# Performance work log

Hardware: AMD Instinct MI355X
Metric: run time of the kernel (lower is better)

## Reference

```python
import jax, jax.numpy as jnp
import numpy as np

D_MODEL = 1024
N_HEADS = 16
D_HEAD = D_MODEL // N_HEADS
NEG_INF = -1000000000.0


def setup_inputs() -> dict:
    key = jax.random.key(0)
    ks = jax.random.split(key, 12)
    B, S1, S2 = 2, 2048, 2048
    query = jax.random.normal(ks[0], (B, S1, D_MODEL), dtype=jnp.float32)
    k_in = jax.random.normal(ks[1], (B, S2, D_MODEL), dtype=jnp.float32)
    v_in = jax.random.normal(ks[2], (B, S2, D_MODEL), dtype=jnp.float32)
    # causal mask: True = position is masked out (filled with -1e9)
    mask = jnp.broadcast_to(jnp.triu(jnp.ones((S1, S2), dtype=bool), k=1), (B, S1, S2))
    s = 1.0 / np.sqrt(D_MODEL)
    W_q = jax.random.uniform(ks[3], (D_MODEL, D_MODEL), jnp.float32, -s, s)
    b_q = jax.random.uniform(ks[4], (D_MODEL,), jnp.float32, -s, s)
    W_k = jax.random.uniform(ks[5], (D_MODEL, D_MODEL), jnp.float32, -s, s)
    b_k = jax.random.uniform(ks[6], (D_MODEL,), jnp.float32, -s, s)
    W_v = jax.random.uniform(ks[7], (D_MODEL, D_MODEL), jnp.float32, -s, s)
    b_v = jax.random.uniform(ks[8], (D_MODEL,), jnp.float32, -s, s)
    W_o = jax.random.uniform(ks[9], (D_MODEL, D_MODEL), jnp.float32, -s, s)
    b_o = jax.random.uniform(ks[10], (D_MODEL,), jnp.float32, -s, s)
    return {"query": query, "key": k_in, "value": v_in, "mask": mask,
            "W_q": W_q, "b_q": b_q, "W_k": W_k, "b_k": b_k,
            "W_v": W_v, "b_v": b_v, "W_o": W_o, "b_o": b_o}


def reference(query, key, value, mask, W_q, b_q, W_k, b_k, W_v, b_v, W_o, b_o):
    B, S1, _ = query.shape
    S2 = key.shape[1]
    scalar = 1.0 / np.sqrt(D_HEAD)
    # projections (torch Linear: x @ W.T + b)
    Q = (query @ W_q.T + b_q).reshape(B, S1, N_HEADS, D_HEAD).transpose(0, 2, 1, 3)
    K = (key @ W_k.T + b_k).reshape(B, S2, N_HEADS, D_HEAD).transpose(0, 2, 1, 3)
    V = (value @ W_v.T + b_v).reshape(B, S2, N_HEADS, D_HEAD).transpose(0, 2, 1, 3)
    # [B, H, S1, S2]
    scores = jnp.einsum('bhqd,bhkd->bhqk', Q, K) * scalar
    scores = jnp.where(mask[:, None, :, :], NEG_INF, scores)
    probs = jax.nn.softmax(scores, axis=-1)
    attn = jnp.einsum('bhqk,bhkd->bhqd', probs, V)
    concat = attn.transpose(0, 2, 1, 3).reshape(B, S1, D_MODEL)
    return concat @ W_o.T + b_o
```

## Files before the change

kernel.cpp:

```cpp
#include <hip/hip_runtime.h>
#include <hip/hip_bf16.h>
#include <stdint.h>

typedef __bf16 bf16;
typedef __bf16 bf16x8 __attribute__((ext_vector_type(8)));
typedef float f32x4 __attribute__((ext_vector_type(4)));
typedef float f32x16 __attribute__((ext_vector_type(16)));
typedef unsigned int u32;
typedef u32 u32x4 __attribute__((ext_vector_type(4)));

#define D_MODEL 1024
#define S_LEN 2048
#define NB 2
#define NH 16
#define DH 64

__device__ __forceinline__ void gload_lds16(const bf16* g, bf16* l) {
    auto gp = reinterpret_cast<const __attribute__((address_space(1))) unsigned int*>(
        reinterpret_cast<uintptr_t>(g));
    auto lp = reinterpret_cast<__attribute__((address_space(3))) unsigned int*>(
        reinterpret_cast<uintptr_t>(l));
    __builtin_amdgcn_global_load_lds(gp, lp, 16, 0, 0);
}

__device__ __forceinline__ u32 cvtpk(float lo, float hi) {
    u32 r; asm("v_cvt_pk_bf16_f32 %0, %1, %2" : "=v"(r) : "v"(lo), "v"(hi)); return r;
}
__device__ __forceinline__ void plswap(u32& a, u32& b) {
    asm("v_permlane32_swap_b32 %0, %1" : "+v"(a), "+v"(b));
}

__global__ __launch_bounds__(256)
void cvt_all(const float* __restrict__ q, const float* __restrict__ k,
             const float* __restrict__ v, const float* __restrict__ w0,
             const float* __restrict__ w1, const float* __restrict__ w2,
             const float* __restrict__ w3,
             bf16* __restrict__ oq, bf16* __restrict__ ok, bf16* __restrict__ ov,
             bf16* __restrict__ o0, bf16* __restrict__ o1, bf16* __restrict__ o2,
             bf16* __restrict__ o3)
{
    const int bid = blockIdx.x;
    const float* in; bf16* out; int local;
    if (bid < 6144) {
        int r = bid >> 11; local = bid & 2047;
        in  = (r == 0) ? q  : (r == 1) ? k  : v;
        out = (r == 0) ? oq : (r == 1) ? ok : ov;
    } else {
        int wb = bid - 6144;
        int r = wb >> 9; local = wb & 511;
        in  = (r == 0) ? w0 : (r == 1) ? w1 : (r == 2) ? w2 : w3;
        out = (r == 0) ? o0 : (r == 1) ? o1 : (r == 2) ? o2 : o3;
    }
    const size_t i = ((size_t)local * 256 + threadIdx.x) * 8;
    f32x4 x = *(const f32x4*)(in + i);
    f32x4 y = *(const f32x4*)(in + i + 4);
    bf16x8 o;
    #pragma unroll
    for (int j = 0; j < 4; ++j) { o[j] = (bf16)x[j]; o[4 + j] = (bf16)y[j]; }
    *(bf16x8*)(out + i) = o;
}

template<int OUT_F32, int TRANS>
__global__ __launch_bounds__(256)
void gemm_bf16(const bf16* __restrict__ Ap, const bf16* __restrict__ Bp,
               const float* __restrict__ bias, void* __restrict__ Cp,
               int M, int N, int K, float cscale)
{
    __shared__ __align__(16) bf16 As[2][128 * 64];
    __shared__ __align__(16) bf16 Bs[2][64 * 64];

    const int t = threadIdx.x, lane = t & 63, wid = t >> 6;
    const int nbn = N >> 6;
    const int cpx = gridDim.x >> 3;
    const int bid = blockIdx.x;
    const int swz = (bid & 7) * cpx + (bid >> 3);
    const int bm0 = (swz / nbn) << 7;
    const int bn0 = (swz % nbn) << 6;
    const int r16 = lane & 15, g = lane >> 4;
    const int wr = (wid >> 1) << 6;
    const int wc = (wid & 1) << 5;

    f32x4 acc[4][2] = {};

    auto stage = [&](int buf, int k0) {
        #pragma unroll
        for (int i = 0; i < 4; ++i) {
            int ch = wid * 256 + i * 64 + lane;
            int row = ch >> 3, c8 = ch & 7;
            int sc = c8 ^ (row & 7);
            gload_lds16(Ap + (size_t)(bm0 + row) * K + k0 + sc * 8, &As[buf][ch * 8]);
        }
        #pragma unroll
        for (int i = 0; i < 2; ++i) {
            int ch = wid * 128 + i * 64 + lane;
            int row = ch >> 3, c8 = ch & 7;
            int sc = c8 ^ (row & 7);
            gload_lds16(Bp + (size_t)(bn0 + row) * K + k0 + sc * 8, &Bs[buf][ch * 8]);
        }
    };

    int cur = 0;
    stage(0, 0);
    for (int k0 = 0; k0 < K; k0 += 64) {
        __syncthreads();
        if (k0 + 64 < K) stage(cur ^ 1, k0 + 64);
        #pragma unroll
        for (int ks = 0; ks < 2; ++ks) {
            const int cl = ks * 4 + g;
            bf16x8 af[4], bfr[2];
            #pragma unroll
            for (int mi = 0; mi < 4; ++mi) {
                int row = wr + mi * 16 + r16;
                af[mi] = *(const bf16x8*)((const char*)&As[cur][0] + row * 128 + ((cl ^ (row & 7)) << 4));
            }
            #pragma unroll
            for (int ni = 0; ni < 2; ++ni) {
                int row = wc + ni * 16 + r16;
                bfr[ni] = *(const bf16x8*)((const char*)&Bs[cur][0] + row * 128 + ((cl ^ (row & 7)) << 4));
            }
            #pragma unroll
            for (int mi = 0; mi < 4; ++mi)
                #pragma unroll
                for (int ni = 0; ni < 2; ++ni)
                    acc[mi][ni] = __builtin_amdgcn_mfma_f32_16x16x32_bf16(af[mi], bfr[ni], acc[mi][ni], 0, 0, 0);
        }
        cur ^= 1;
    }

    const int rb = g * 4;
    if (TRANS) {
        __syncthreads();
        bf16* Ts = (bf16*)&As[0][0];
        #pragma unroll
        for (int mi = 0; mi < 4; ++mi)
            #pragma unroll
            for (int ni = 0; ni < 2; ++ni) {
                int dl = wc + ni * 16 + r16;
                float bv = bias[bn0 + dl];
                #pragma unroll
                for (int r = 0; r < 4; ++r) {
                    int sl = wr + mi * 16 + rb + r;
                    Ts[dl * 136 + sl] = (bf16)(acc[mi][ni][r] + bv);
                }
            }
        __syncthreads();
        const int bq = bm0 >> 11, hq = bn0 >> 6, s0 = bm0 & 2047;
        bf16* VT = (bf16*)Cp;
        #pragma unroll
        for (int i2 = 0; i2 < 4; ++i2) {
            int ch = t + i2 * 256;
            int d = ch >> 4, sc = ch & 15;
            bf16x8 v = *(const bf16x8*)&Ts[d * 136 + sc * 8];
            *(bf16x8*)(VT + ((size_t)(bq * 16 + hq) * 64 + d) * S_LEN + s0 + sc * 8) = v;
        }
    } else {
        #pragma unroll
        for (int mi = 0; mi < 4; ++mi) {
            #pragma unroll
            for (int ni = 0; ni < 2; ++ni) {
                int cg = bn0 + wc + ni * 16 + r16;
                float bv = bias[cg];
                #pragma unroll
                for (int r = 0; r < 4; ++r) {
                    int rg = bm0 + wr + mi * 16 + rb + r;
                    float v = (acc[mi][ni][r] + bv) * cscale;
                    if (OUT_F32) ((float*)Cp)[(size_t)rg * N + cg] = v;
                    else         ((bf16*)Cp)[(size_t)rg * N + cg] = (bf16)v;
                }
            }
        }
    }
}

__global__ __launch_bounds__(512, 2)
void attn4(const bf16* __restrict__ Qp, const bf16* __restrict__ Kp,
           const bf16* __restrict__ VTp, bf16* __restrict__ Op)
{
    __shared__ __align__(16) char smem[66560];

    const int t = threadIdx.x, lane = t & 63, wid = t >> 6;
    const int l31 = lane & 31, hh = lane >> 5;
    const int qs = wid & 3, ks2 = wid >> 2;

    const int bid = blockIdx.x;
    const int xcd = bid & 7, idx = bid >> 3;
    const int bh = xcd * 4 + (idx >> 3);
    const int pr = idx & 7;
    const int b = bh >> 4, h = bh & 15;

    const size_t base = (size_t)b * (S_LEN * D_MODEL) + h * DH;
    const size_t vtbase = (size_t)bh * (DH * S_LEN);

    const int ch = wid * 64 + lane;
    const int srow = ch >> 3, sc8 = ch & 7;
    const int ssc = (sc8 ^ (srow & 7)) << 3;

    #pragma unroll 1
    for (int ph = 0; ph < 2; ++ph) {
        const int qtile = ph ? (15 - pr) : pr;
        const int half = qtile + 1;
        const int q0b = qtile * 128;
        const int q0w = q0b + qs * 32;
        const int tmask0 = 2 * qtile + (qs >> 1);
        const int teff = tmask0 + 1;

        bf16x8 qf[4];
        {
            const bf16* qrow = Qp + base + (size_t)(q0w + l31) * D_MODEL + hh * 8;
            #pragma unroll
            for (int db = 0; db < 4; ++db) qf[db] = *(const bf16x8*)(qrow + db * 16);
        }

        f32x16 oacc[2] = {};
        float mx = -1e30f, lsum = 0.f;

        auto stage = [&](int buf, int tA, int tB) {
            gload_lds16(Kp + base + (size_t)(tA * 64 + srow) * D_MODEL + ssc,
                        (bf16*)(smem + ((0 * 2 + buf) * 2 + 0) * 8192 + ch * 16));
            gload_lds16(VTp + vtbase + (size_t)srow * S_LEN + tA * 64 + ssc,
                        (bf16*)(smem + ((0 * 2 + buf) * 2 + 1) * 8192 + ch * 16));
            gload_lds16(Kp + base + (size_t)(tB * 64 + srow) * D_MODEL + ssc,
                        (bf16*)(smem + ((1 * 2 + buf) * 2 + 0) * 8192 + ch * 16));
            gload_lds16(VTp + vtbase + (size_t)srow * S_LEN + tB * 64 + ssc,
                        (bf16*)(smem + ((1 * 2 + buf) * 2 + 1) * 8192 + ch * 16));
        };

        int cur = 0;
        stage(0, 0, half);
        #pragma unroll 1
        for (int r = 0; r < half; ++r) {
            __syncthreads();
            if (r + 1 < half) stage(cur ^ 1, r + 1, half + r + 1);
            const int tt = ks2 ? (half + r) : r;
            if (tt < teff) {
                const char* kbp = smem + ((ks2 * 2 + cur) * 2 + 0) * 8192;
                const char* vbp = smem + ((ks2 * 2 + cur) * 2 + 1) * 8192;
                f32x16 sacc[2] = {};
                #pragma unroll
                for (int ks = 0; ks < 2; ++ks)
                    #pragma unroll
                    for (int db = 0; db < 4; ++db) {
                        int row = ks * 32 + l31, c = db * 2 + hh;
                        bf16x8 kf = *(const bf16x8*)(kbp + row * 128 + ((c ^ (row & 7)) << 4));
                        sacc[ks] = __builtin_amdgcn_mfma_f32_32x32x16_bf16(kf, qf[db], sacc[ks], 0, 0, 0);
                    }
                bf16x8 vf[8];
                #pragma unroll
                for (int kb2 = 0; kb2 < 4; ++kb2)
                    #pragma unroll
                    for (int dt = 0; dt < 2; ++dt) {
                        int row = dt * 32 + l31, c = kb2 * 2 + hh;
                        vf[kb2 * 2 + dt] = *(const bf16x8*)(vbp + row * 128 + ((c ^ (row & 7)) << 4));
                    }
                if (tt >= tmask0) {
                    const int thr = q0w + l31 - 4 * hh - tt * 64;
                    #pragma unroll
                    for (int ks = 0; ks < 2; ++ks)
                        #pragma unroll
                        for (int r2 = 0; r2 < 16; ++r2) {
                            const int cr = 32 * ks + (r2 & 3) + 8 * (r2 >> 2);
                            if (cr > thr) sacc[ks][r2] = -1e9f;
                        }
                }
                float pm = -3e38f;
                #pragma unroll
                for (int ks = 0; ks < 2; ++ks)
                    #pragma unroll
                    for (int r2 = 0; r2 < 16; ++r2) pm = fmaxf(pm, sacc[ks][r2]);
                pm = fmaxf(pm, __shfl_xor(pm, 32));
                float mnew = fmaxf(mx, pm);
                float al = __builtin_exp2f(mx - mnew);
                float ts = 0.f;
                #pragma unroll
                for (int ks = 0; ks < 2; ++ks)
                    #pragma unroll
                    for (int r2 = 0; r2 < 16; ++r2) {
                        float p = __builtin_exp2f(sacc[ks][r2] - mnew);
                        sacc[ks][r2] = p;
                        ts += p;
                    }
                ts += __shfl_xor(ts, 32);
                lsum = lsum * al + ts;
                mx = mnew;
                #pragma unroll
                for (int dt = 0; dt < 2; ++dt)
                    #pragma unroll
                    for (int r2 = 0; r2 < 16; ++r2) oacc[dt][r2] *= al;

                #pragma unroll
                for (int kb2 = 0; kb2 < 4; ++kb2) {
                    const int ks = kb2 >> 1, rb2 = (kb2 & 1) * 8;
                    u32 w0 = cvtpk(sacc[ks][rb2 + 0], sacc[ks][rb2 + 1]);
                    u32 w2 = cvtpk(sacc[ks][rb2 + 4], sacc[ks][rb2 + 5]);
                    u32 w1 = cvtpk(sacc[ks][rb2 + 2], sacc[ks][rb2 + 3]);
                    u32 w3 = cvtpk(sacc[ks][rb2 + 6], sacc[ks][rb2 + 7]);
                    plswap(w0, w2);
                    plswap(w1, w3);
                    u32x4 pw; pw[0] = w0; pw[1] = w1; pw[2] = w2; pw[3] = w3;
                    bf16x8 pb = __builtin_bit_cast(bf16x8, pw);
                    #pragma unroll
                    for (int dt = 0; dt < 2; ++dt)
                        oacc[dt] = __builtin_amdgcn_mfma_f32_32x32x16_bf16(vf[kb2 * 2 + dt], pb, oacc[dt], 0, 0, 0);
                }
            }
            cur ^= 1;
        }

        __syncthreads();
        float* mlS = (float*)(smem + 65536);
        if (ks2 == 1) {
            float* Of = (float*)(smem + qs * 8192);
            #pragma unroll
            for (int dt = 0; dt < 2; ++dt)
                #pragma unroll
                for (int r2 = 0; r2 < 16; ++r2) {
                    int d = dt * 32 + (r2 & 3) + 8 * (r2 >> 2) + 4 * hh;
                    Of[d * 32 + l31] = oacc[dt][r2];
                }
            if (hh == 0) { mlS[qs * 64 + l31] = mx; mlS[qs * 64 + 32 + l31] = lsum; }
        }
        __syncthreads();
        if (ks2 == 0) {
            float m1 = mlS[qs * 64 + l31], l1 = mlS[qs * 64 + 32 + l31];
            float m = fmaxf(mx, m1);
            float a0 = __builtin_exp2f(mx - m), a1 = __builtin_exp2f(m1 - m);
            float linv = 1.0f / (lsum * a0 + l1 * a1);
            a0 *= linv; a1 *= linv;
            const float* Of = (const float*)(smem + qs * 8192);
            char* Os = smem + 32768 + qs * 4352;
            #pragma unroll
            for (int dt = 0; dt < 2; ++dt)
                #pragma unroll
                for (int r2 = 0; r2 < 16; r2 += 2) {
                    int d = dt * 32 + (r2 & 3) + 8 * (r2 >> 2) + 4 * hh;
                    float o0 = oacc[dt][r2]     * a0 + Of[d * 32 + l31]       * a1;
                    float o1 = oacc[dt][r2 + 1] * a0 + Of[(d + 1) * 32 + l31] * a1;
                    *(u32*)(Os + l31 * 136 + d * 2) = cvtpk(o0, o1);
                }
        }
        __syncthreads();
        #pragma unroll
        for (int i2 = 0; i2 < 2; ++i2) {
            int ch2 = t + i2 * 512;
            int qrow = ch2 >> 3, c8 = ch2 & 7;
            bf16x8 v = *(const bf16x8*)(smem + 32768 + (qrow >> 5) * 4352 + (qrow & 31) * 136 + c8 * 16);
            *(bf16x8*)(Op + base + (size_t)(q0b + qrow) * D_MODEL + c8 * 8) = v;
        }
        __syncthreads();
    }
}

extern "C" void kernel_launch(void* const* d_in, const int* in_sizes, int n_in,
                              void* d_out, int out_size, void* d_ws, size_t ws_size,
                              hipStream_t stream)
{
    const float* query = (const float*)d_in[0];
    const float* key   = (const float*)d_in[1];
    const float* value = (const float*)d_in[2];
    const float* W_q = (const float*)d_in[4];
    const float* b_q = (const float*)d_in[5];
    const float* W_k = (const float*)d_in[6];
    const float* b_k = (const float*)d_in[7];
    const float* W_v = (const float*)d_in[8];
    const float* b_v = (const float*)d_in[9];
    const float* W_o = (const float*)d_in[10];
    const float* b_o = (const float*)d_in[11];

    const int M = NB * S_LEN;
    char* w = (char*)d_ws;
    const size_t MB = 1 << 20;
    bf16* qbf = (bf16*)(w);
    bf16* kbf = (bf16*)(w + 8 * MB);
    bf16* vbf = (bf16*)(w + 16 * MB);
    bf16* Qb  = (bf16*)(w + 24 * MB);
    bf16* Kb  = (bf16*)(w + 32 * MB);
    bf16* VT  = (bf16*)(w + 40 * MB);
    bf16* Wqb = (bf16*)(w + 48 * MB);
    bf16* Wkb = (bf16*)(w + 50 * MB);
    bf16* Wvb = (bf16*)(w + 52 * MB);
    bf16* Wob = (bf16*)(w + 54 * MB);
    bf16* Ob  = qbf;

    dim3 blk(256);
    cvt_all<<<dim3(8192), blk, 0, stream>>>(query, key, value, W_q, W_k, W_v, W_o,
                                            qbf, kbf, vbf, Wqb, Wkb, Wvb, Wob);

    dim3 gproj((M / 128) * (D_MODEL / 64));
    const float qscale = 0.125f * 1.4426950408889634f;
    gemm_bf16<0, 0><<<gproj, blk, 0, stream>>>(qbf, Wqb, b_q, Qb, M, D_MODEL, D_MODEL, qscale);
    gemm_bf16<0, 0><<<gproj, blk, 0, stream>>>(kbf, Wkb, b_k, Kb, M, D_MODEL, D_MODEL, 1.0f);
    gemm_bf16<0, 1><<<gproj, blk, 0, stream>>>(vbf, Wvb, b_v, VT, M, D_MODEL, D_MODEL, 1.0f);

    attn4<<<dim3(256), dim3(512), 0, stream>>>(Qb, Kb, VT, Ob);

    gemm_bf16<1, 0><<<gproj, blk, 0, stream>>>(Ob, Wob, b_o, d_out, M, D_MODEL, D_MODEL, 1.0f);
}
```

Measured before the change: 111.1 us.

## Replace split-KV paired-tile attention with one-q-tile-per-block causal scheduling

The attention kernel used 512-thread blocks that handled two paired q-tiles in sequence and split the KV range across two wave groups, merging the halves through shared memory. It now launches 512 blocks of 256 threads. Each block processes one 128-row q tile over its full causal KV range, with heaviest tiles scheduled first, and finalises directly with 1/lsum. This removes the split-KV merge and the extra syncs and halves shared memory per block, which may allow more resident blocks. It also adds s_setprio around the MFMA sections, but per-block work is now unbalanced and each wave runs a longer serial KV loop.

```diff
diff --git a/kernel.cpp b/kernel.cpp
--- a/kernel.cpp
+++ b/kernel.cpp
@@ -172,181 +172,157 @@
     }
 }
 
-__global__ __launch_bounds__(512, 2)
-void attn4(const bf16* __restrict__ Qp, const bf16* __restrict__ Kp,
+__global__ __launch_bounds__(256, 2)
+void attn5(const bf16* __restrict__ Qp, const bf16* __restrict__ Kp,
            const bf16* __restrict__ VTp, bf16* __restrict__ Op)
 {
-    __shared__ __align__(16) char smem[66560];
-
-    const int t = threadIdx.x, lane = t & 63, wid = t >> 6;
+    __shared__ __align__(16) char smem[32768];
+
+    const int t = threadIdx.x, lane = t & 63, qs = t >> 6;
     const int l31 = lane & 31, hh = lane >> 5;
-    const int qs = wid & 3, ks2 = wid >> 2;
 
     const int bid = blockIdx.x;
-    const int xcd = bid & 7, idx = bid >> 3;
-    const int bh = xcd * 4 + (idx >> 3);
-    const int pr = idx & 7;
+    const int xcd = bid & 7, slot = bid >> 3;
+    const int bh = xcd * 4 + (slot & 3);
+    const int sh = slot >> 2;
+    const int qt = (sh < 8) ? (15 - sh) : (sh - 8);
     const int b = bh >> 4, h = bh & 15;
 
     const size_t base = (size_t)b * (S_LEN * D_MODEL) + h * DH;
     const size_t vtbase = (size_t)bh * (DH * S_LEN);
 
-    const int ch = wid * 64 + lane;
-    const int srow = ch >> 3, sc8 = ch & 7;
-    const int ssc = (sc8 ^ (srow & 7)) << 3;
-
+    const int q0b = qt * 128;
+    const int q0w = q0b + qs * 32;
+    const int NT = 2 * qt + 2;
+    const int teff = 2 * qt + (qs >> 1) + 1;
+
+    const int ch0 = t, ch1 = t + 256;
+    const int row0 = ch0 >> 3, ssc0 = ((ch0 & 7) ^ (row0 & 7)) << 3;
+    const int row1 = ch1 >> 3, ssc1 = ((ch1 & 7) ^ (row1 & 7)) << 3;
+
+    auto stage = [&](int buf, int tt) {
+        char* kb = smem + buf * 16384;
+        char* vb = kb + 8192;
+        gload_lds16(Kp + base + (size_t)(tt * 64 + row0) * D_MODEL + ssc0, (bf16*)(kb + ch0 * 16));
+        gload_lds16(Kp + base + (size_t)(tt * 64 + row1) * D_MODEL + ssc1, (bf16*)(kb + ch1 * 16));
+        gload_lds16(VTp + vtbase + (size_t)row0 * S_LEN + tt * 64 + ssc0, (bf16*)(vb + ch0 * 16));
+        gload_lds16(VTp + vtbase + (size_t)row1 * S_LEN + tt * 64 + ssc1, (bf16*)(vb + ch1 * 16));
+    };
+
+    bf16x8 qf[4];
+    {
+        const bf16* qrow = Qp + base + (size_t)(q0w + l31) * D_MODEL + hh * 8;
+        #pragma unroll
+        for (int db = 0; db < 4; ++db) qf[db] = *(const bf16x8*)(qrow + db * 16);
+    }
+
+    f32x16 oacc[2] = {};
+    float mx = -1e30f, lsum = 0.f;
+
+    int cur = 0;
+    stage(0, 0);
     #pragma unroll 1
-    for (int ph = 0; ph < 2; ++ph) {
-        const int qtile = ph ? (15 - pr) : pr;
-        const int half = qtile + 1;
-        const int q0b = qtile * 128;
-        const int q0w = q0b + qs * 32;
-        const int tmask0 = 2 * qtile + (qs >> 1);
-        const int teff = tmask0 + 1;
-
-        bf16x8 qf[4];
-        {
-            const bf16* qrow = Qp + base + (size_t)(q0w + l31) * D_MODEL + hh * 8;
-            #pragma unroll
-            for (int db = 0; db < 4; ++db) qf[db] = *(const bf16x8*)(qrow + db * 16);
-        }
-
-        f32x16 oacc[2] = {};
-        float mx = -1e30f, lsum = 0.f;
-
-        auto stage = [&](int buf, int tA, int tB) {
-            gload_lds16(Kp + base + (size_t)(tA * 64 + srow) * D_MODEL + ssc,
-                        (bf16*)(smem + ((0 * 2 + buf) * 2 + 0) * 8192 + ch * 16));
-            gload_lds16(VTp + vtbase + (size_t)srow * S_LEN + tA * 64 + ssc,
-                        (bf16*)(smem + ((0 * 2 + buf) * 2 + 1) * 8192 + ch * 16));
-            gload_lds16(Kp + base + (size_t)(tB * 64 + srow) * D_MODEL + ssc,
-                        (bf16*)(smem + ((1 * 2 + buf) * 2 + 0) * 8192 + ch * 16));
-            gload_lds16(VTp + vtbase + (size_t)srow * S_LEN + tB * 64 + ssc,
-                        (bf16*)(smem + ((1 * 2 + buf) * 2 + 1) * 8192 + ch * 16));
-        };
-
-        int cur = 0;
-        stage(0, 0, half);
-        #pragma unroll 1
-        for (int r = 0; r < half; ++r) {
-            __syncthreads();
-            if (r + 1 < half) stage(cur ^ 1, r + 1, half + r + 1);
-            const int tt = ks2 ? (half + r) : r;
-            if (tt < teff) {
-                const char* kbp = smem + ((ks2 * 2 + cur) * 2 + 0) * 8192;
-                const char* vbp = smem + ((ks2 * 2 + cur) * 2 + 1) * 8192;
-                f32x16 sacc[2] = {};
-                #pragma unroll
-                for (int ks = 0; ks < 2; ++ks)
-                    #pragma unroll
-                    for (int db = 0; db < 4; ++db) {
-                        int row = ks * 32 + l31, c = db * 2 + hh;
-                        bf16x8 kf = *(const bf16x8*)(kbp + row * 128 + ((c ^ (row & 7)) << 4));
-                        sacc[ks] = __builtin_amdgcn_mfma_f32_32x32x16_bf16(kf, qf[db], sacc[ks], 0, 0, 0);
-                    }
-                bf16x8 vf[8];
-                #pragma unroll
-                for (int kb2 = 0; kb2 < 4; ++kb2)
-                    #pragma unroll
-                    for (int dt = 0; dt < 2; ++dt) {
-                        int row = dt * 32 + l31, c = kb2 * 2 + hh;
-                        vf[kb2 * 2 + dt] = *(const bf16x8*)(vbp + row * 128 + ((c ^ (row & 7)) << 4));
-                    }
-                if (tt >= tmask0) {
-                    const int thr = q0w + l31 - 4 * hh - tt * 64;
-                    #pragma unroll
-                    for (int ks = 0; ks < 2; ++ks)
-                        #pragma unroll
-                        for (int r2 = 0; r2 < 16; ++r2) {
-                            const int cr = 32 * ks + (r2 & 3) + 8 * (r2 >> 2);
-                            if (cr > thr) sacc[ks][r2] = -1e9f;
-                        }
-                }
-                float pm = -3e38f;
-                #pragma unroll
-                for (int ks = 0; ks < 2; ++ks)
-                    #pragma unroll
-                    for (int r2 = 0; r2 < 16; ++r2) pm = fmaxf(pm, sacc[ks][r2]);
-                pm = fmaxf(pm, __shfl_xor(pm, 32));
-                float mnew = fmaxf(mx, pm);
-                float al = __builtin_exp2f(mx - mnew);
-                float ts = 0.f;
+    for (int tt = 0; tt < NT; ++tt) {
+        __syncthreads();
+        if (tt + 1 < NT) stage(cur ^ 1, tt + 1);
+        if (tt < teff) {
+            const char* kbp = smem + cur * 16384;
+            const char* vbp = kbp + 8192;
+            f32x16 sacc[2] = {};
+            __builtin_amdgcn_s_setprio(1);
+            #pragma unroll
+            for (int ks = 0; ks < 2; ++ks)
+                #pragma unroll
+                for (int db = 0; db < 4; ++db) {
+                    int row = ks * 32 + l31, c = db * 2 + hh;
+                    bf16x8 kf = *(const bf16x8*)(kbp + row * 128 + ((c ^ (row & 7)) << 4));
+                    sacc[ks] = __builtin_amdgcn_mfma_f32_32x32x16_bf16(kf, qf[db], sacc[ks], 0, 0, 0);
+                }
+            __builtin_amdgcn_s_setprio(0);
+            bf16x8 vf[8];
+            #pragma unroll
+            for (int kb2 = 0; kb2 < 4; ++kb2)
+                #pragma unroll
+                for (int dt = 0; dt < 2; ++dt) {
+                    int row = dt * 32 + l31, c = kb2 * 2 + hh;
+                    vf[kb2 * 2 + dt] = *(const bf16x8*)(vbp + row * 128 + ((c ^ (row & 7)) << 4));
+                }
+            if (tt == teff - 1) {
+                const int thr = q0w + l31 - 4 * hh - tt * 64;
                 #pragma unroll
                 for (int ks = 0; ks < 2; ++ks)
                     #pragma unroll
                     for (int r2 = 0; r2 < 16; ++r2) {
-                        float p = __builtin_exp2f(sacc[ks][r2] - mnew);
-                        sacc[ks][r2] = p;
-                        ts += p;
+                        const int cr = 32 * ks + (r2 & 3) + 8 * (r2 >> 2);
+                        if (cr > thr) sacc[ks][r2] = -1e9f;
                     }
-                ts += __shfl_xor(ts, 32);
-                lsum = lsum * al + ts;
-                mx = mnew;
+            }
+            float pm = -3e38f;
+            #pragma unroll
+            for (int ks = 0; ks < 2; ++ks)
+                #pragma unroll
+                for (int r2 = 0; r2 < 16; ++r2) pm = fmaxf(pm, sacc[ks][r2]);
+            pm = fmaxf(pm, __shfl_xor(pm, 32));
+            float mnew = fmaxf(mx, pm);
+            float al = __builtin_exp2f(mx - mnew);
+            float ts = 0.f;
+            #pragma unroll
+            for (int ks = 0; ks < 2; ++ks)
+                #pragma unroll
+                for (int r2 = 0; r2 < 16; ++r2) {
+                    float p = __builtin_exp2f(sacc[ks][r2] - mnew);
+                    sacc[ks][r2] = p;
+                    ts += p;
+                }
+            ts += __shfl_xor(ts, 32);
+            lsum = lsum * al + ts;
+            mx = mnew;
+            #pragma unroll
+            for (int dt = 0; dt < 2; ++dt)
+                #pragma unroll
+                for (int r2 = 0; r2 < 16; ++r2) oacc[dt][r2] *= al;
+
+            #pragma unroll
+            for (int kb2 = 0; kb2 < 4; ++kb2) {
+                const int ks = kb2 >> 1, rb2 = (kb2 & 1) * 8;
+                u32 w0 = cvtpk(sacc[ks][rb2 + 0], sacc[ks][rb2 + 1]);
+                u32 w2 = cvtpk(sacc[ks][rb2 + 4], sacc[ks][rb2 + 5]);
+                u32 w1 = cvtpk(sacc[ks][rb2 + 2], sacc[ks][rb2 + 3]);
+                u32 w3 = cvtpk(sacc[ks][rb2 + 6], sacc[ks][rb2 + 7]);
+                plswap(w0, w2);
+                plswap(w1, w3);
+                u32x4 pw; pw[0] = w0; pw[1] = w1; pw[2] = w2; pw[3] = w3;
+                bf16x8 pb = __builtin_bit_cast(bf16x8, pw);
+                __builtin_amdgcn_s_setprio(1);
                 #pragma unroll
                 for (int dt = 0; dt < 2; ++dt)
-                    #pragma unroll
-                    for (int r2 = 0; r2 < 16; ++r2) oacc[dt][r2] *= al;
-
-                #pragma unroll
-                for (int kb2 = 0; kb2 < 4; ++kb2) {
-                    const int ks = kb2 >> 1, rb2 = (kb2 & 1) * 8;
-                    u32 w0 = cvtpk(sacc[ks][rb2 + 0], sacc[ks][rb2 + 1]);
-                    u32 w2 = cvtpk(sacc[ks][rb2 + 4], sacc[ks][rb2 + 5]);
-                    u32 w1 = cvtpk(sacc[ks][rb2 + 2], sacc[ks][rb2 + 3]);
-                    u32 w3 = cvtpk(sacc[ks][rb2 + 6], sacc[ks][rb2 + 7]);
-                    plswap(w0, w2);
-                    plswap(w1, w3);
-                    u32x4 pw; pw[0] = w0; pw[1] = w1; pw[2] = w2; pw[3] = w3;
-                    bf16x8 pb = __builtin_bit_cast(bf16x8, pw);
-                    #pragma unroll
-                    for (int dt = 0; dt < 2; ++dt)
-                        oacc[dt] = __builtin_amdgcn_mfma_f32_32x32x16_bf16(vf[kb2 * 2 + dt], pb, oacc[dt], 0, 0, 0);
-                }
-            }
-            cur ^= 1;
-        }
-
-        __syncthreads();
-        float* mlS = (float*)(smem + 65536);
-        if (ks2 == 1) {
-            float* Of = (float*)(smem + qs * 8192);
-            #pragma unroll
-            for (int dt = 0; dt < 2; ++dt)
-                #pragma unroll
-                for (int r2 = 0; r2 < 16; ++r2) {
-                    int d = dt * 32 + (r2 & 3) + 8 * (r2 >> 2) + 4 * hh;
-                    Of[d * 32 + l31] = oacc[dt][r2];
-                }
-            if (hh == 0) { mlS[qs * 64 + l31] = mx; mlS[qs * 64 + 32 + l31] = lsum; }
-        }
-        __syncthreads();
-        if (ks2 == 0) {
-            float m1 = mlS[qs * 64 + l31], l1 = mlS[qs * 64 + 32 + l31];
-            float m = fmaxf(mx, m1);
-            float a0 = __builtin_exp2f(mx - m), a1 = __builtin_exp2f(m1 - m);
-            float linv = 1.0f / (lsum * a0 + l1 * a1);
-            a0 *= linv; a1 *= linv;
-            const float* Of = (const float*)(smem + qs * 8192);
-            char* Os = smem + 32768 + qs * 4352;
-            #pragma unroll
-            for (int dt = 0; dt < 2; ++dt)
-                #pragma unroll
-                for (int r2 = 0; r2 < 16; r2 += 2) {
-                    int d = dt * 32 + (r2 & 3) + 8 * (r2 >> 2) + 4 * hh;
-                    float o0 = oacc[dt][r2]     * a0 + Of[d * 32 + l31]       * a1;
-                    float o1 = oacc[dt][r2 + 1] * a0 + Of[(d + 1) * 32 + l31] * a1;
-                    *(u32*)(Os + l31 * 136 + d * 2) = cvtpk(o0, o1);
-                }
-        }
-        __syncthreads();
-        #pragma unroll
-        for (int i2 = 0; i2 < 2; ++i2) {
-            int ch2 = t + i2 * 512;
-            int qrow = ch2 >> 3, c8 = ch2 & 7;
-            bf16x8 v = *(const bf16x8*)(smem + 32768 + (qrow >> 5) * 4352 + (qrow & 31) * 136 + c8 * 16);
-            *(bf16x8*)(Op + base + (size_t)(q0b + qrow) * D_MODEL + c8 * 8) = v;
-        }
-        __syncthreads();
+                    oacc[dt] = __builtin_amdgcn_mfma_f32_32x32x16_bf16(vf[kb2 * 2 + dt], pb, oacc[dt], 0, 0, 0);
+                __builtin_amdgcn_s_setprio(0);
+            }
+        }
+        cur ^= 1;
+    }
+
+    __syncthreads();
+    {
+        const float inv = 1.0f / lsum;
+        char* Os = smem;
+        #pragma unroll
+        for (int dt = 0; dt < 2; ++dt)
+            #pragma unroll
+            for (int r2 = 0; r2 < 16; r2 += 2) {
+                int d = dt * 32 + (r2 & 3) + 8 * (r2 >> 2) + 4 * hh;
+                u32 w = cvtpk(oacc[dt][r2] * inv, oacc[dt][r2 + 1] * inv);
+                *(u32*)(Os + (qs * 32 + l31) * 136 + d * 2) = w;
+            }
+    }
+    __syncthreads();
+    #pragma unroll
+    for (int i2 = 0; i2 < 4; ++i2) {
+        int ch2 = t + i2 * 256;
+        int qrow = ch2 >> 3, c8 = ch2 & 7;
+        bf16x8 v = *(const bf16x8*)(smem + qrow * 136 + c8 * 16);
+        *(bf16x8*)(Op + base + (size_t)(q0b + qrow) * D_MODEL + c8 * 8) = v;
     }
 }
 
@@ -391,7 +367,7 @@
     gemm_bf16<0, 0><<<gproj, blk, 0, stream>>>(kbf, Wkb, b_k, Kb, M, D_MODEL, D_MODEL, 1.0f);
     gemm_bf16<0, 1><<<gproj, blk, 0, stream>>>(vbf, Wvb, b_v, VT, M, D_MODEL, D_MODEL, 1.0f);
 
-    attn4<<<dim3(256), dim3(512), 0, stream>>>(Qb, Kb, VT, Ob);
+    attn5<<<dim3(512), blk, 0, stream>>>(Qb, Kb, VT, Ob);
 
     gemm_bf16<1, 0><<<gproj, blk, 0, stream>>>(Ob, Wob, b_o, d_out, M, D_MODEL, D_MODEL, 1.0f);
 }
```

Measured after the change: 115.2 us. 3.7% more time.
